# Optimization experiments

Measured on AMD Instinct MI355X. Metric: run time of the kernel, lower is better.

The kernel has to match this reference:

```python
import jax, jax.numpy as jnp
import numpy as np

LAMBDA_WEIGHT = 1.0


def _soft_argmax(logits):
    # differentiable_argmax: sum_c softmax(logits)[c] * c along class dim
    nc = logits.shape[1]
    probs = jax.nn.softmax(logits, axis=1)
    idx = jnp.arange(nc, dtype=logits.dtype)[None, :, None, None]
    return jnp.sum(probs * idx, axis=1)  # [B, H, W]


def _pair_loss(mask, d):
    # mask: [L] bool over row-major flattened HxW; d: [L] float (col - row).
    # torch.where returns row-major order, coord[:,1]-coord[:,0] == d at masked
    # pixels; second diff is |d_i - d_prev| over consecutive masked pixels.
    L = mask.shape[0]
    pos = jnp.where(mask, jnp.arange(L), -1)
    last = jax.lax.cummax(pos, axis=0)                 # last masked index <= i
    prev = jnp.concatenate([jnp.full((1,), -1), last[:-1]])  # strictly before i
    valid = mask & (prev >= 0)
    dprev = d[jnp.clip(prev, 0, L - 1)]
    s = jnp.sum(jnp.where(valid, jnp.abs(d - dprev), 0.0))
    npairs = jnp.sum(valid)
    npts = jnp.sum(mask)
    mean = s / jnp.maximum(npairs, 1).astype(d.dtype)
    # N==0 contributes 0 (the `continue`); N==1 gives an empty-mean (NaN) in
    # torch -- guarded to 0 here (such degenerate classes are skipped).
    return jnp.where(npts >= 2, mean / (npts + 1).astype(d.dtype), 0.0)


def reference(logits, labels):
    bs, nc, h, w = logits.shape
    seg = jnp.floor(jax.lax.stop_gradient(_soft_argmax(logits))).astype(jnp.int32)
    seg = seg.reshape(bs, h * w)                       # [B, L] row-major
    # d[i] = col - row for flattened index i
    i = jnp.arange(h * w)
    d = ((i % w) - (i // w)).astype(jnp.float32)       # [L]
    classes = jnp.arange(1, nc, dtype=jnp.int32)       # skip background c=0
    masks = seg[:, None, :] == classes[None, :, None]  # [B, nc-1, L]
    per = jax.vmap(jax.vmap(_pair_loss, in_axes=(0, None)), in_axes=(0, None))(masks, d)
    return jnp.sum(per) * LAMBDA_WEIGHT


def setup_inputs() -> dict:
    key = jax.random.key(0)
    k1, k2 = jax.random.split(key)
    logits = jax.random.normal(k1, (16, 7, 368, 640), dtype=jnp.float32)
    labels = jax.random.randint(k2, (16, 368, 640), 0, 7, dtype=jnp.int64)
    return {"logits": logits, "labels": labels}
```

## Files before the change

kernel.cpp:

```cpp
#include <hip/hip_runtime.h>
#include <cstdint>
#include <cstddef>

#define BB 16
#define CC 7
#define HH 368
#define WW 640
#define LL (HH * WW)
#define NCLS 6
#define NCOMBO (BB * NCLS)
#define NROWS (BB * HH)
#define RPB 4
#define NBLK (NROWS / RPB)

typedef float v4f __attribute__((ext_vector_type(4)));

__device__ inline v4f ntload4(const float* p) {
    return __builtin_nontemporal_load(reinterpret_cast<const v4f*>(p));
}

__global__ __launch_bounds__(256) void rowstat_kernel(const float* __restrict__ logits,
                                                      int4* __restrict__ rowStats) {
    int t    = threadIdx.x;
    int w    = t >> 6;
    int lane = t & 63;
    int grow = blockIdx.x * RPB + w;
    int b = grow / HH;
    int r = grow - b * HH;
    const float* rowbase = logits + (size_t)b * CC * LL + (size_t)r * WW;

    float sacc[12], wacc[12];
#pragma unroll
    for (int k = 0; k < 12; ++k) { sacc[k] = 0.0f; wacc[k] = 0.0f; }

#pragma unroll
    for (int c = 0; c < CC; ++c) {
        const float* p = rowbase + (size_t)c * LL;
        v4f a = ntload4(p + lane * 4);
        v4f bq = ntload4(p + 256 + lane * 4);
        v4f cq = (lane < 32) ? ntload4(p + 512 + lane * 4) : v4f{0, 0, 0, 0};
        float xv[12] = {a.x, a.y, a.z, a.w, bq.x, bq.y, bq.z, bq.w,
                        cq.x, cq.y, cq.z, cq.w};
#pragma unroll
        for (int k = 0; k < 12; ++k) {
            float e = __expf(xv[k]);
            sacc[k] += e;
            wacc[k] += e * (float)c;
        }
    }

    int cnt[NCLS], mn[NCLS], mx[NCLS];
#pragma unroll
    for (int c = 0; c < NCLS; ++c) { cnt[c] = 0; mn[c] = 1 << 30; mx[c] = -1; }

#pragma unroll
    for (int k = 0; k < 12; ++k) {
        if (k >= 8 && lane >= 32) break;
        int sv  = (int)floorf(__fdividef(wacc[k], sacc[k]));
        int col = (k < 4) ? (lane * 4 + k)
                          : (k < 8) ? (256 + lane * 4 + (k - 4))
                                    : (512 + lane * 4 + (k - 8));
#pragma unroll
        for (int c = 0; c < NCLS; ++c) {
            int m = (sv == c + 1);
            cnt[c] += m;
            mn[c] = m ? min(mn[c], col) : mn[c];
            mx[c] = m ? max(mx[c], col) : mx[c];
        }
    }

#pragma unroll
    for (int c = 0; c < NCLS; ++c) {
        if (__ballot(cnt[c] > 0) == 0ull) { cnt[c] = 0; continue; }
#pragma unroll
        for (int off = 1; off < 64; off <<= 1) {
            cnt[c] += __shfl_down(cnt[c], off, 64);
            mn[c]  = min(mn[c], __shfl_down(mn[c], off, 64));
            mx[c]  = max(mx[c], __shfl_down(mx[c], off, 64));
        }
    }

    if (lane == 0) {
#pragma unroll
        for (int c = 0; c < NCLS; ++c)
            rowStats[(size_t)(b * NCLS + c) * HH + r] = make_int4(cnt[c], mn[c], mx[c], 0);
    }
}

struct St { int S, cnt, first, last; };

__device__ inline St comb(const St& a, const St& b) {
    St r;
    int both = (a.cnt > 0) & (b.cnt > 0);
    r.S     = a.S + b.S + (both ? abs(b.first - a.last) : 0);
    r.cnt   = a.cnt + b.cnt;
    r.first = (a.cnt > 0) ? a.first : b.first;
    r.last  = (b.cnt > 0) ? b.last : a.last;
    return r;
}

__device__ inline St shfl_down_st(const St& s, int off) {
    St r;
    r.S     = __shfl_down(s.S, off, 64);
    r.cnt   = __shfl_down(s.cnt, off, 64);
    r.first = __shfl_down(s.first, off, 64);
    r.last  = __shfl_down(s.last, off, 64);
    return r;
}

__global__ __launch_bounds__(256) void combine_kernel(const int4* __restrict__ rowStats,
                                                      float* __restrict__ out) {
    int combo = blockIdx.x;
    int t = threadIdx.x;
    const int4* rp = rowStats + (size_t)combo * HH;

    St st{0, 0, 0, 0};
    if (t < HH / 2) {
#pragma unroll
        for (int q = 0; q < 2; ++q) {
            int row = 2 * t + q;
            int4 v = rp[row];
            if (v.x > 0) {
                St rs{v.z - v.y, v.x, v.y - row, v.z - row};
                st = comb(st, rs);
            }
        }
    }

#pragma unroll
    for (int off = 1; off < 64; off <<= 1) {
        St o = shfl_down_st(st, off);
        st = comb(st, o);
    }

    __shared__ int4 ws[4];
    int wave = t >> 6;
    if ((t & 63) == 0) ws[wave] = make_int4(st.S, st.cnt, st.first, st.last);
    __syncthreads();

    if (t == 0) {
        St acc{ws[0].x, ws[0].y, ws[0].z, ws[0].w};
#pragma unroll
        for (int q = 1; q < 4; ++q) {
            St o{ws[q].x, ws[q].y, ws[q].z, ws[q].w};
            acc = comb(acc, o);
        }
        int n = acc.cnt;
        if (n >= 2) {
            double res = ((double)acc.S / (double)(n - 1)) / (double)(n + 1);
            atomicAdd(out, (float)res);
        }
    }
}

extern "C" void kernel_launch(void* const* d_in, const int* in_sizes, int n_in,
                              void* d_out, int out_size, void* d_ws, size_t ws_size,
                              hipStream_t stream) {
    const float* logits = (const float*)d_in[0];
    float* out = (float*)d_out;

    int4* rowStats = (int4*)d_ws;

    hipMemsetAsync(out, 0, sizeof(float) * out_size, stream);
    rowstat_kernel<<<NBLK, 256, 0, stream>>>(logits, rowStats);
    combine_kernel<<<NCOMBO, 256, 0, stream>>>(rowStats, out);
}
```

Before: 162.2 us.

## Split class channels across waves per row pair and reduce via LDS

Each block now handles two image rows. Its four waves each load a disjoint subset of class channels (2,2,2,1) for both rows and write partial softmax sums to shared memory. After a barrier, each thread combines the four partials for 5 pixels, computes the soft-argmax class and reduces count/min/max per wave, then merges wave pairs into per-row stats. This raises the number of independent loads in flight per wave. It adds LDS traffic, two barriers, an unbalanced final wave, and drops the nontemporal load hint.

```diff
diff --git a/kernel.cpp b/kernel.cpp
--- a/kernel.cpp
+++ b/kernel.cpp
@@ -9,57 +9,86 @@
 #define LL (HH * WW)
 #define NCLS 6
 #define NCOMBO (BB * NCLS)
-#define NROWS (BB * HH)
-#define RPB 4
-#define NBLK (NROWS / RPB)
-
-typedef float v4f __attribute__((ext_vector_type(4)));
-
-__device__ inline v4f ntload4(const float* p) {
-    return __builtin_nontemporal_load(reinterpret_cast<const v4f*>(p));
-}
+#define PAIRS_PB (HH / 2)
+#define NPAIRS (BB * PAIRS_PB)
 
 __global__ __launch_bounds__(256) void rowstat_kernel(const float* __restrict__ logits,
                                                       int4* __restrict__ rowStats) {
+    __shared__ float sArr[4][1280];
+    __shared__ float wArr[4][1280];
+    __shared__ int wcnt[4][NCLS], wmn[4][NCLS], wmx[4][NCLS];
+
     int t    = threadIdx.x;
     int w    = t >> 6;
     int lane = t & 63;
-    int grow = blockIdx.x * RPB + w;
-    int b = grow / HH;
-    int r = grow - b * HH;
-    const float* rowbase = logits + (size_t)b * CC * LL + (size_t)r * WW;
-
-    float sacc[12], wacc[12];
-#pragma unroll
-    for (int k = 0; k < 12; ++k) { sacc[k] = 0.0f; wacc[k] = 0.0f; }
-
-#pragma unroll
-    for (int c = 0; c < CC; ++c) {
-        const float* p = rowbase + (size_t)c * LL;
-        v4f a = ntload4(p + lane * 4);
-        v4f bq = ntload4(p + 256 + lane * 4);
-        v4f cq = (lane < 32) ? ntload4(p + 512 + lane * 4) : v4f{0, 0, 0, 0};
-        float xv[12] = {a.x, a.y, a.z, a.w, bq.x, bq.y, bq.z, bq.w,
-                        cq.x, cq.y, cq.z, cq.w};
-#pragma unroll
-        for (int k = 0; k < 12; ++k) {
-            float e = __expf(xv[k]);
-            sacc[k] += e;
-            wacc[k] += e * (float)c;
-        }
-    }
+    int pid  = blockIdx.x;
+    int b  = pid / PAIRS_PB;
+    int r0 = (pid - b * PAIRS_PB) * 2;
+    const float* pairbase = logits + (size_t)b * CC * LL + (size_t)r0 * WW;
+
+    if (w < 3) {
+        int c0 = w * 2;
+        const float* p0 = pairbase + (size_t)c0 * LL;
+        const float* p1 = pairbase + (size_t)(c0 + 1) * LL;
+        float4 a[5], bq[5];
+#pragma unroll
+        for (int it = 0; it < 5; ++it)
+            a[it] = *reinterpret_cast<const float4*>(p0 + it * 256 + lane * 4);
+#pragma unroll
+        for (int it = 0; it < 5; ++it)
+            bq[it] = *reinterpret_cast<const float4*>(p1 + it * 256 + lane * 4);
+        float f0 = (float)c0, f1 = (float)(c0 + 1);
+#pragma unroll
+        for (int it = 0; it < 5; ++it) {
+            float4 sv, wv;
+            float e0, e1;
+            e0 = __expf(a[it].x); e1 = __expf(bq[it].x);
+            sv.x = e0 + e1; wv.x = e0 * f0 + e1 * f1;
+            e0 = __expf(a[it].y); e1 = __expf(bq[it].y);
+            sv.y = e0 + e1; wv.y = e0 * f0 + e1 * f1;
+            e0 = __expf(a[it].z); e1 = __expf(bq[it].z);
+            sv.z = e0 + e1; wv.z = e0 * f0 + e1 * f1;
+            e0 = __expf(a[it].w); e1 = __expf(bq[it].w);
+            sv.w = e0 + e1; wv.w = e0 * f0 + e1 * f1;
+            int px = it * 256 + lane * 4;
+            *reinterpret_cast<float4*>(&sArr[w][px]) = sv;
+            *reinterpret_cast<float4*>(&wArr[w][px]) = wv;
+        }
+    } else {
+        const float* p0 = pairbase + (size_t)6 * LL;
+        float4 a[5];
+#pragma unroll
+        for (int it = 0; it < 5; ++it)
+            a[it] = *reinterpret_cast<const float4*>(p0 + it * 256 + lane * 4);
+#pragma unroll
+        for (int it = 0; it < 5; ++it) {
+            float4 sv, wv;
+            sv.x = __expf(a[it].x); wv.x = sv.x * 6.0f;
+            sv.y = __expf(a[it].y); wv.y = sv.y * 6.0f;
+            sv.z = __expf(a[it].z); wv.z = sv.z * 6.0f;
+            sv.w = __expf(a[it].w); wv.w = sv.w * 6.0f;
+            int px = it * 256 + lane * 4;
+            *reinterpret_cast<float4*>(&sArr[w][px]) = sv;
+            *reinterpret_cast<float4*>(&wArr[w][px]) = wv;
+        }
+    }
+    __syncthreads();
+
+    int px0 = t * 5;
+    int row = w >> 1;
+    int colbase = px0 - row * WW;
 
     int cnt[NCLS], mn[NCLS], mx[NCLS];
 #pragma unroll
     for (int c = 0; c < NCLS; ++c) { cnt[c] = 0; mn[c] = 1 << 30; mx[c] = -1; }
 
 #pragma unroll
-    for (int k = 0; k < 12; ++k) {
-        if (k >= 8 && lane >= 32) break;
-        int sv  = (int)floorf(__fdividef(wacc[k], sacc[k]));
-        int col = (k < 4) ? (lane * 4 + k)
-                          : (k < 8) ? (256 + lane * 4 + (k - 4))
-                                    : (512 + lane * 4 + (k - 8));
+    for (int j = 0; j < 5; ++j) {
+        int px = px0 + j;
+        float s    = (sArr[0][px] + sArr[1][px]) + (sArr[2][px] + sArr[3][px]);
+        float wsum = (wArr[0][px] + wArr[1][px]) + (wArr[2][px] + wArr[3][px]);
+        int sv  = (int)floorf(__fdividef(wsum, s));
+        int col = colbase + j;
 #pragma unroll
         for (int c = 0; c < NCLS; ++c) {
             int m = (sv == c + 1);
@@ -79,11 +108,21 @@
             mx[c]  = max(mx[c], __shfl_down(mx[c], off, 64));
         }
     }
-
     if (lane == 0) {
 #pragma unroll
-        for (int c = 0; c < NCLS; ++c)
-            rowStats[(size_t)(b * NCLS + c) * HH + r] = make_int4(cnt[c], mn[c], mx[c], 0);
+        for (int c = 0; c < NCLS; ++c) {
+            wcnt[w][c] = cnt[c]; wmn[w][c] = mn[c]; wmx[w][c] = mx[c];
+        }
+    }
+    __syncthreads();
+
+    if (t < 2 * NCLS) {
+        int R = t / NCLS, c = t - R * NCLS;
+        int w0 = 2 * R, w1 = 2 * R + 1;
+        int C  = wcnt[w0][c] + wcnt[w1][c];
+        int Mn = min(wmn[w0][c], wmn[w1][c]);
+        int Mx = max(wmx[w0][c], wmx[w1][c]);
+        rowStats[(size_t)(b * NCLS + c) * HH + r0 + R] = make_int4(C, Mn, Mx, 0);
     }
 }
 
@@ -162,6 +201,6 @@
     int4* rowStats = (int4*)d_ws;
 
     hipMemsetAsync(out, 0, sizeof(float) * out_size, stream);
-    rowstat_kernel<<<NBLK, 256, 0, stream>>>(logits, rowStats);
+    rowstat_kernel<<<NPAIRS, 256, 0, stream>>>(logits, rowStats);
     combine_kernel<<<NCOMBO, 256, 0, stream>>>(rowStats, out);
 }
```

Result: no change. 164.8 us (+1.6%).
